# Kernel optimization log

Hardware: AMD Instinct MI355X
Metric: run time of the kernel (lower is better)

## Reference

```python
import jax, jax.numpy as jnp
import numpy as np

B, C, H, W = 2048, 512, 4, 4
T, D, NH, HD, FF, NL = 16, 512, 8, 64, 1024, 4
EPS = 1e-5
SCALE = float(1.0 / np.sqrt(HD))


def _make_adj(h, w):
    # torch_geometric.utils.grid(h, w): 3x3 neighborhood incl. self-loop;
    # GCNConv sym-normalizes: A_hat = D^-1/2 A D^-1/2
    n = h * w
    A = np.zeros((n, n), np.float32)
    for r in range(h):
        for c in range(w):
            for dr in (-1, 0, 1):
                for dc in (-1, 0, 1):
                    rr, cc = r + dr, c + dc
                    if 0 <= rr < h and 0 <= cc < w:
                        A[r * w + c, rr * w + cc] = 1.0
    dinv = 1.0 / np.sqrt(A.sum(1))
    return (A * dinv[:, None] * dinv[None, :]).astype(np.float32)


def setup_inputs():
    key = jax.random.key(0)
    ks = iter(jax.random.split(key, 64))
    def w(*s):
        return jax.random.normal(next(ks), s, jnp.float32) * 0.02
    return dict(
        x=jax.random.normal(next(ks), (B, C, H, W), jnp.float32),
        emb_w=w(D, D), emb_b=jnp.zeros((D,), jnp.float32),
        emb_ln_g=jnp.ones((D,), jnp.float32), emb_ln_b=jnp.zeros((D,), jnp.float32),
        pos=w(1, T, D),
        attn_wq=w(NL, D, D), attn_wk=w(NL, D, D), attn_wv=w(NL, D, D),
        attn_bq=jnp.zeros((NL, D), jnp.float32), attn_bk=jnp.zeros((NL, D), jnp.float32),
        attn_bv=jnp.zeros((NL, D), jnp.float32),
        attn_wo=w(NL, D, D), attn_bo=jnp.zeros((NL, D), jnp.float32),
        ln1_g=jnp.ones((NL, D), jnp.float32), ln1_b=jnp.zeros((NL, D), jnp.float32),
        ff_w1=w(NL, D, FF), ff_b1=jnp.zeros((NL, FF), jnp.float32),
        ff_w2=w(NL, FF, D), ff_b2=jnp.zeros((NL, D), jnp.float32),
        ln2_g=jnp.ones((NL, D), jnp.float32), ln2_b=jnp.zeros((NL, D), jnp.float32),
        fc_w=w(D, D), fc_b=jnp.zeros((D,), jnp.float32),
        fc_ln_g=jnp.ones((D,), jnp.float32), fc_ln_b=jnp.zeros((D,), jnp.float32),
        gcn_w1=w(C, 2 * C), gcn_b1=jnp.zeros((2 * C,), jnp.float32),
        gcn_ln1_g=jnp.ones((2 * C,), jnp.float32), gcn_ln1_b=jnp.zeros((2 * C,), jnp.float32),
        gcn_w2=w(2 * C, C), gcn_b2=jnp.zeros((C,), jnp.float32),
        gcn_ln2_g=jnp.ones((C,), jnp.float32), gcn_ln2_b=jnp.zeros((C,), jnp.float32),
        fusion_w=w(C, 2 * C), fusion_b=jnp.zeros((C,), jnp.float32),
        adj=jnp.asarray(_make_adj(H, W)),
    )


def _ln(x, g, b):
    mu = x.mean(-1, keepdims=True)
    var = ((x - mu) ** 2).mean(-1, keepdims=True)
    return (x - mu) * jax.lax.rsqrt(var + EPS) * g + b


def reference(x, emb_w, emb_b, emb_ln_g, emb_ln_b, pos,
              attn_wq, attn_wk, attn_wv, attn_bq, attn_bk, attn_bv, attn_wo, attn_bo,
              ln1_g, ln1_b, ff_w1, ff_b1, ff_w2, ff_b2, ln2_g, ln2_b,
              fc_w, fc_b, fc_ln_g, fc_ln_b,
              gcn_w1, gcn_b1, gcn_ln1_g, gcn_ln1_b, gcn_w2, gcn_b2, gcn_ln2_g, gcn_ln2_b,
              fusion_w, fusion_b, adj):
    Bx = x.shape[0]
    # ---- transformer branch: tokens = 16 spatial positions, dim 512 ----
    h = x.reshape(Bx, C, T).transpose(0, 2, 1)                 # [B,T,D]
    h = _ln(h @ emb_w + emb_b, emb_ln_g, emb_ln_b) + pos
    for i in range(NL):  # post-norm TransformerEncoderLayer, ReLU, eval (no dropout)
        q = (h @ attn_wq[i] + attn_bq[i]).reshape(Bx, T, NH, HD).transpose(0, 2, 1, 3)
        k = (h @ attn_wk[i] + attn_bk[i]).reshape(Bx, T, NH, HD).transpose(0, 2, 1, 3)
        v = (h @ attn_wv[i] + attn_bv[i]).reshape(Bx, T, NH, HD).transpose(0, 2, 1, 3)
        a = jax.nn.softmax(jnp.einsum('bhqd,bhkd->bhqk', q, k) * SCALE, axis=-1)
        o = jnp.einsum('bhqk,bhkd->bhqd', a, v).transpose(0, 2, 1, 3).reshape(Bx, T, D)
        h = _ln(h + o @ attn_wo[i] + attn_bo[i], ln1_g[i], ln1_b[i])
        f = jax.nn.relu(h @ ff_w1[i] + ff_b1[i]) @ ff_w2[i] + ff_b2[i]
        h = _ln(h + f, ln2_g[i], ln2_b[i])
    h = _ln(h @ fc_w + fc_b, fc_ln_g, fc_ln_b)
    x1 = h.transpose(0, 2, 1).reshape(Bx, C, H, W)
    # ---- GCN branch: dense normalized adjacency over the 16-node grid ----
    xn = x.transpose(0, 2, 3, 1).reshape(Bx, T, C)             # [B,16,C]
    g = jnp.einsum('mn,bnd->bmd', adj, xn @ gcn_w1) + gcn_b1   # GCNConv1 (bias after aggr)
    g = jax.nn.elu(_ln(g, gcn_ln1_g, gcn_ln1_b))
    g = jnp.einsum('mn,bnd->bmd', adj, g @ gcn_w2) + gcn_b2    # GCNConv2
    g = jax.nn.elu(_ln(g, gcn_ln2_g, gcn_ln2_b))
    x2 = g.reshape(Bx, H, W, C).transpose(0, 3, 1, 2)
    # ---- fusion: 1x1 conv + InstanceNorm2d (no affine) + ELU ----
    xc = jnp.concatenate([x1, x2], axis=1)                     # [B,2C,H,W]
    y = jnp.einsum('oc,bchw->bohw', fusion_w, xc) + fusion_b[None, :, None, None]
    mu = y.mean((2, 3), keepdims=True)
    var = ((y - mu) ** 2).mean((2, 3), keepdims=True)
    y = (y - mu) * jax.lax.rsqrt(var + EPS)
    return jax.nn.elu(y)
```

## Files before the change

### kernel.cpp

```cpp
#include <hip/hip_runtime.h>


typedef _Float16 f16;
typedef f16 f16x8 __attribute__((ext_vector_type(8)));
typedef f16 f16x4 __attribute__((ext_vector_type(4)));
typedef float f32x4 __attribute__((ext_vector_type(4)));

#define BM 128
#define BN 128
#define BK 32

__device__ inline float wred_sum(float s) {
#pragma unroll
  for (int m = 32; m; m >>= 1) s += __shfl_xor(s, m);
  return s;
}

struct WDesc {
  const float* src;
  f16* dst;
  int K, N, tiles_n, tile_base, mode;
};
struct WTable {
  WDesc d[32];
  int n;
};

__global__ void wconvert_kernel(WTable tab) {
  const int tile = blockIdx.x;
  int di = 0;
  while (di + 1 < tab.n && tab.d[di + 1].tile_base <= tile) ++di;
  const WDesc w = tab.d[di];
  const int t = tile - w.tile_base;
  const int tk = t / w.tiles_n, tn = t % w.tiles_n;
  const int tid = threadIdx.x;
  const int rr = tid >> 5, cc = tid & 31;
  __shared__ float tb[32][33];
  if (w.mode == 0) {
#pragma unroll
    for (int i = 0; i < 4; i++) {
      const int k = tk * 32 + i * 8 + rr, n = tn * 32 + cc;
      tb[i * 8 + rr][cc] = w.src[(size_t)k * w.N + n];
    }
    __syncthreads();
#pragma unroll
    for (int i = 0; i < 4; i++) {
      const int n = tn * 32 + i * 8 + rr, k = tk * 32 + cc;
      w.dst[(size_t)n * w.K + k] = (f16)tb[cc][i * 8 + rr];
    }
  } else {
#pragma unroll
    for (int i = 0; i < 4; i++) {
      const int k = tk * 32 + i * 8 + rr, n = tn * 32 + cc;
      w.dst[(size_t)k * w.N + n] = (f16)w.src[(size_t)k * w.N + n];
    }
  }
}

__global__ void biaspack_kernel(const float* __restrict__ bq,
                                const float* __restrict__ bk,
                                const float* __restrict__ bv,
                                float* __restrict__ bqkv) {
  const int i = blockIdx.x * 256 + threadIdx.x;
  if (i >= 4 * 1536) return;
  const int l = i / 1536, j = i % 1536;
  float v;
  if (j < 512)       v = bq[l * 512 + j];
  else if (j < 1024) v = bk[l * 512 + j - 512];
  else               v = bv[l * 512 + j - 1024];
  bqkv[i] = v;
}

__global__ void prep_kernel(const float* __restrict__ x, f16* __restrict__ X0) {
  const int b = blockIdx.x;
  for (int c = threadIdx.x; c < 512; c += 256) {
    const float* src = x + ((size_t)b * 512 + c) * 16;
    float vals[16];
#pragma unroll
    for (int i = 0; i < 4; i++) {
      const float4 v = ((const float4*)src)[i];
      vals[i * 4 + 0] = v.x; vals[i * 4 + 1] = v.y;
      vals[i * 4 + 2] = v.z; vals[i * 4 + 3] = v.w;
    }
#pragma unroll
    for (int t = 0; t < 16; t++)
      X0[((size_t)b * 16 + t) * 512 + c] = (f16)vals[t];
  }
}

template <int OUT, bool RELU, bool HASB>
__global__ __launch_bounds__(256) void gemm_kernel(
    const f16* __restrict__ A, const f16* __restrict__ Bt, void* __restrict__ C,
    const float* __restrict__ bias, int N, int K, int lda, int ldb) {
  __shared__ alignas(16) f16 sm[3][8192];
  const int tid = threadIdx.x;
  const int nb = N >> 7;
  const int cpx = gridDim.x >> 3;
  const int wg = (blockIdx.x & 7) * cpx + (blockIdx.x >> 3);
  const int bx = wg % nb;
  const int by = wg / nb;
  const int row0 = by << 7, col0 = bx << 7;
  const int lane = tid & 63;
  const int wave = tid >> 6;
  const int wm = (wave >> 1) << 6;
  const int wn = (wave & 1) << 6;
  const int srow = tid >> 2;
  const int schunk = (tid & 3) ^ ((tid >> 3) & 3);
  const f16* gA = A + (size_t)(row0 + srow) * lda + (schunk << 3);
  const f16* gB = Bt + (size_t)(col0 + srow) * ldb + (schunk << 3);
  const int wave_off = (tid & 0xC0) << 3;
  f32x4 acc[4][4] = {};
  const int rm = lane & 15;
  const int kg = lane >> 4;
  const int nt = K >> 5;

  auto STAGE = [&](int t, int bufi) {
    f16* lA = sm[bufi] + wave_off;
    f16* lB = sm[bufi] + 4096 + wave_off;
    const int kt = t << 5;
    __builtin_amdgcn_global_load_lds(
        (const __attribute__((address_space(1))) void*)(gA + kt),
        (__attribute__((address_space(3))) void*)lA, 16, 0, 0);
    __builtin_amdgcn_global_load_lds(
        (const __attribute__((address_space(1))) void*)(gA + (size_t)64 * lda + kt),
        (__attribute__((address_space(3))) void*)(lA + 2048), 16, 0, 0);
    __builtin_amdgcn_global_load_lds(
        (const __attribute__((address_space(1))) void*)(gB + kt),
        (__attribute__((address_space(3))) void*)lB, 16, 0, 0);
    __builtin_amdgcn_global_load_lds(
        (const __attribute__((address_space(1))) void*)(gB + (size_t)64 * ldb + kt),
        (__attribute__((address_space(3))) void*)(lB + 2048), 16, 0, 0);
  };

  STAGE(0, 0);
  STAGE(1, 1);
  asm volatile("s_waitcnt vmcnt(4)" ::: "memory");
  __builtin_amdgcn_s_barrier();

  for (int t = 0; t < nt; ++t) {
    const int cur = t % 3;
    if (t + 2 < nt) STAGE(t + 2, (t + 2) % 3);
    const f16* As = sm[cur];
    const f16* Bs = sm[cur] + 4096;
    f16x8 af[4], bf[4];
#pragma unroll
    for (int m = 0; m < 4; ++m) {
      const int r = wm + m * 16 + rm;
      af[m] = *(const f16x8*)(As + (r << 5) + ((kg ^ ((r >> 1) & 3)) << 3));
    }
#pragma unroll
    for (int n = 0; n < 4; ++n) {
      const int r = wn + n * 16 + rm;
      bf[n] = *(const f16x8*)(Bs + (r << 5) + ((kg ^ ((r >> 1) & 3)) << 3));
    }
#pragma unroll
    for (int m = 0; m < 4; ++m)
#pragma unroll
      for (int n = 0; n < 4; ++n)
        acc[m][n] =
            __builtin_amdgcn_mfma_f32_16x16x32_f16(af[m], bf[n], acc[m][n], 0, 0, 0);
    if (t + 2 < nt) {
      asm volatile("s_waitcnt vmcnt(4)" ::: "memory");
    } else {
      asm volatile("s_waitcnt vmcnt(0)" ::: "memory");
    }
    __builtin_amdgcn_s_barrier();
  }

  const int cn = lane & 15;
  const int rg = (lane >> 4) << 2;
#pragma unroll
  for (int m = 0; m < 4; ++m) {
#pragma unroll
    for (int n = 0; n < 4; ++n) {
      const int col = col0 + wn + n * 16 + cn;
      const float bv = HASB ? bias[col] : 0.0f;
#pragma unroll
      for (int r = 0; r < 4; ++r) {
        const int row = row0 + wm + m * 16 + rg + r;
        float v = acc[m][n][r] + bv;
        if (OUT == 2) v += ((float*)C)[(size_t)row * N + col];
        if (RELU) v = v > 0.f ? v : 0.f;
        if (OUT == 0)
          ((f16*)C)[(size_t)row * N + col] = (f16)v;
        else
          ((float*)C)[(size_t)row * N + col] = v;
      }
    }
  }
}

template <bool RES, bool POS>
__global__ void ln_kernel(const f16* in, const f16* res, const float* g,
                          const float* b, const float* pos, f16* out) {
  const int row = (blockIdx.x << 2) + (threadIdx.x >> 6);
  const int lane = threadIdx.x & 63;
  const int c0 = lane << 3;
  float v[8];
  const f16x8 xi = *(const f16x8*)(in + (size_t)row * 512 + c0);
  if (RES) {
    const f16x8 ri = *(const f16x8*)(res + (size_t)row * 512 + c0);
#pragma unroll
    for (int j = 0; j < 8; j++) v[j] = (float)xi[j] + (float)ri[j];
  } else {
#pragma unroll
    for (int j = 0; j < 8; j++) v[j] = (float)xi[j];
  }
  float s = 0;
#pragma unroll
  for (int j = 0; j < 8; j++) s += v[j];
  s = wred_sum(s);
  const float mu = s * (1.f / 512.f);
  float q = 0;
#pragma unroll
  for (int j = 0; j < 8; j++) {
    const float d = v[j] - mu;
    q += d * d;
  }
  q = wred_sum(q);
  const float rstd = rsqrtf(q * (1.f / 512.f) + 1e-5f);
  const int t = row & 15;
  f16x8 o8;
#pragma unroll
  for (int j = 0; j < 8; j++) {
    float o = (v[j] - mu) * rstd * g[c0 + j] + b[c0 + j];
    if (POS) o += pos[t * 512 + c0 + j];
    o8[j] = (f16)o;
  }
  *(f16x8*)(out + (size_t)row * 512 + c0) = o8;
}

__global__ __launch_bounds__(256) void attn_kernel(const f16* __restrict__ qkv,
                                                   f16* __restrict__ o) {
  __shared__ f16 smem[4][3776];
  const int wid = threadIdx.x >> 6;
  const int lane = threadIdx.x & 63;
  const int bh = (blockIdx.x << 2) + wid;
  const int b = bh >> 3, h = bh & 7;
  f16* W = smem[wid];
  f16* Qw = W;
  f16* Kw = W + 1152;
  f16* Vw = W + 2304;
  f16* Pw = W + 3456;
  const size_t base = (size_t)b * 24576 + (size_t)h * 64;
#pragma unroll
  for (int i = 0; i < 6; i++) {
    const int c = i * 64 + lane;
    const int t = c / 24;
    const int rem = c - t * 24;
    const int mat = rem >> 3, ch = rem & 7;
    const f16x8 v = *(const f16x8*)(qkv + base + (size_t)t * 1536 + mat * 512 + ch * 8);
    *(f16x8*)(W + mat * 1152 + t * 72 + ch * 8) = v;
  }
  __syncthreads();
  const int rm = lane & 15, kg = lane >> 4;
  f32x4 s4 = {};
  {
    const f16x8 q0 = *(const f16x8*)(Qw + rm * 72 + kg * 8);
    const f16x8 q1 = *(const f16x8*)(Qw + rm * 72 + 32 + kg * 8);
    const f16x8 k0 = *(const f16x8*)(Kw + rm * 72 + kg * 8);
    const f16x8 k1 = *(const f16x8*)(Kw + rm * 72 + 32 + kg * 8);
    s4 = __builtin_amdgcn_mfma_f32_16x16x32_f16(q0, k0, s4, 0, 0, 0);
    s4 = __builtin_amdgcn_mfma_f32_16x16x32_f16(q1, k1, s4, 0, 0, 0);
  }
  float p[4];
#pragma unroll
  for (int r = 0; r < 4; r++) {
    const float sv = s4[r] * 0.125f;
    float m = sv;
    m = fmaxf(m, __shfl_xor(m, 1));
    m = fmaxf(m, __shfl_xor(m, 2));
    m = fmaxf(m, __shfl_xor(m, 4));
    m = fmaxf(m, __shfl_xor(m, 8));
    const float e = expf(sv - m);
    float s = e;
    s += __shfl_xor(s, 1);
    s += __shfl_xor(s, 2);
    s += __shfl_xor(s, 4);
    s += __shfl_xor(s, 8);
    p[r] = e / s;
  }
#pragma unroll
  for (int r = 0; r < 4; r++) Pw[(kg * 4 + r) * 20 + rm] = (f16)p[r];
  __syncthreads();
  const f16x4 pa = *(const f16x4*)(Pw + rm * 20 + kg * 4);
  f32x4 o4[4] = {};
#pragma unroll
  for (int dt = 0; dt < 4; dt++) {
    f16x4 vb;
#pragma unroll
    for (int kk = 0; kk < 4; kk++) vb[kk] = Vw[(kg * 4 + kk) * 72 + dt * 16 + rm];
    o4[dt] = __builtin_amdgcn_mfma_f32_16x16x16f16(pa, vb, o4[dt], 0, 0, 0);
  }
  f16* op = o + (size_t)b * 16 * 512 + (size_t)h * 64;
#pragma unroll
  for (int dt = 0; dt < 4; dt++)
#pragma unroll
    for (int r = 0; r < 4; r++)
      op[(size_t)(kg * 4 + r) * 512 + dt * 16 + rm] = (f16)o4[dt][r];
}

template <int DG>
__global__ __launch_bounds__(256) void adjmix_kernel(
    const f16* __restrict__ r, const float* __restrict__ adj,
    const float* __restrict__ bias, const float* __restrict__ g,
    const float* __restrict__ bet, f16* __restrict__ out, int ldo) {
  const int b = blockIdx.x;
  const int tid = threadIdx.x;
  __shared__ float agg[16][DG];
  __shared__ float adjs[256];
  if (tid < 256) adjs[tid] = adj[tid];
  __syncthreads();
  const int d0 = tid * 4;
  if (d0 < DG) {
    float acc[16][4];
#pragma unroll
    for (int m = 0; m < 16; m++)
#pragma unroll
      for (int j = 0; j < 4; j++) acc[m][j] = 0.f;
#pragma unroll
    for (int n = 0; n < 16; n++) {
      const f16x4 v = *(const f16x4*)(r + ((size_t)b * 16 + n) * DG + d0);
      const float v0 = (float)v[0], v1 = (float)v[1], v2 = (float)v[2], v3 = (float)v[3];
#pragma unroll
      for (int m = 0; m < 16; m++) {
        const float a = adjs[m * 16 + n];
        acc[m][0] += a * v0;
        acc[m][1] += a * v1;
        acc[m][2] += a * v2;
        acc[m][3] += a * v3;
      }
    }
    const float4 bv = *(const float4*)(bias + d0);
#pragma unroll
    for (int m = 0; m < 16; m++) {
      agg[m][d0 + 0] = acc[m][0] + bv.x;
      agg[m][d0 + 1] = acc[m][1] + bv.y;
      agg[m][d0 + 2] = acc[m][2] + bv.z;
      agg[m][d0 + 3] = acc[m][3] + bv.w;
    }
  }
  __syncthreads();
  const int wave = tid >> 6, lane = tid & 63;
  for (int m = wave; m < 16; m += 4) {
    float s = 0;
#pragma unroll
    for (int j = 0; j < DG / 64; j++) s += agg[m][j * 64 + lane];
    s = wred_sum(s);
    const float mu = s / DG;
    float q = 0;
#pragma unroll
    for (int j = 0; j < DG / 64; j++) {
      const float t = agg[m][j * 64 + lane] - mu;
      q += t * t;
    }
    q = wred_sum(q);
    const float rstd = rsqrtf(q / DG + 1e-5f);
    const size_t grow = (size_t)b * 16 + m;
#pragma unroll
    for (int j = 0; j < DG / 64; j++) {
      const int d = j * 64 + lane;
      float v = (agg[m][d] - mu) * rstd * g[d] + bet[d];
      v = v > 0.f ? v : expm1f(v);
      out[grow * ldo + d] = (f16)v;
    }
  }
}

__global__ void instnorm_kernel(const float* __restrict__ y, float* __restrict__ out) {
  const int b = blockIdx.x;
  for (int oc = threadIdx.x; oc < 512; oc += 256) {
    float v[16];
    float s = 0;
#pragma unroll
    for (int t = 0; t < 16; t++) {
      v[t] = y[((size_t)b * 16 + t) * 512 + oc];
      s += v[t];
    }
    const float mu = s * (1.f / 16.f);
    float q = 0;
#pragma unroll
    for (int t = 0; t < 16; t++) {
      const float d = v[t] - mu;
      q += d * d;
    }
    const float rstd = rsqrtf(q * (1.f / 16.f) + 1e-5f);
    float* op = out + ((size_t)b * 512 + oc) * 16;
#pragma unroll
    for (int t = 0; t < 16; t++) {
      const float z = (v[t] - mu) * rstd;
      op[t] = z > 0.f ? z : expm1f(z);
    }
  }
}

extern "C" void kernel_launch(void* const* d_in, const int* in_sizes, int n_in,
                              void* d_out, int out_size, void* d_ws, size_t ws_size,
                              hipStream_t stream) {
  (void)in_sizes; (void)n_in; (void)out_size; (void)ws_size;
  const float* x         = (const float*)d_in[0];
  const float* emb_w     = (const float*)d_in[1];
  const float* emb_b     = (const float*)d_in[2];
  const float* emb_ln_g  = (const float*)d_in[3];
  const float* emb_ln_b  = (const float*)d_in[4];
  const float* pos       = (const float*)d_in[5];
  const float* attn_wq   = (const float*)d_in[6];
  const float* attn_wk   = (const float*)d_in[7];
  const float* attn_wv   = (const float*)d_in[8];
  const float* attn_bq   = (const float*)d_in[9];
  const float* attn_bk   = (const float*)d_in[10];
  const float* attn_bv   = (const float*)d_in[11];
  const float* attn_wo   = (const float*)d_in[12];
  const float* attn_bo   = (const float*)d_in[13];
  const float* ln1_g     = (const float*)d_in[14];
  const float* ln1_b     = (const float*)d_in[15];
  const float* ff_w1     = (const float*)d_in[16];
  const float* ff_b1     = (const float*)d_in[17];
  const float* ff_w2     = (const float*)d_in[18];
  const float* ff_b2     = (const float*)d_in[19];
  const float* ln2_g     = (const float*)d_in[20];
  const float* ln2_b     = (const float*)d_in[21];
  const float* fc_w      = (const float*)d_in[22];
  const float* fc_b      = (const float*)d_in[23];
  const float* fc_ln_g   = (const float*)d_in[24];
  const float* fc_ln_b   = (const float*)d_in[25];
  const float* gcn_w1    = (const float*)d_in[26];
  const float* gcn_b1    = (const float*)d_in[27];
  const float* gcn_ln1_g = (const float*)d_in[28];
  const float* gcn_ln1_b = (const float*)d_in[29];
  const float* gcn_w2    = (const float*)d_in[30];
  const float* gcn_b2    = (const float*)d_in[31];
  const float* gcn_ln2_g = (const float*)d_in[32];
  const float* gcn_ln2_b = (const float*)d_in[33];
  const float* fusion_w  = (const float*)d_in[34];
  const float* fusion_b  = (const float*)d_in[35];
  const float* adj       = (const float*)d_in[36];

  char* ws = (char*)d_ws;
  f16*   WF   = (f16*)(ws);
  float* BQKV = (float*)(ws + 20971520ull);
  f16*   Ap   = (f16*)(ws + 20996096ull);
  f16*   Bp   = (f16*)(ws + 54550528ull);
  f16*   Cp   = (f16*)(ws + 88104960ull);
  f16*   Qp   = (f16*)(ws + 121659392ull);

  const size_t o_emb = 0, o_qkv = 262144, o_wo = 3407872, o_ff1 = 4456448,
               o_ff2 = 6553600, o_fc = 8650752, o_g1 = 8912896, o_g2 = 9437184,
               o_fus = 9961472;

  WTable tab{};
  int ntab = 0, tbase = 0;
  auto add = [&](const float* s, f16* dst, int K, int N, int mode) {
    WDesc& w = tab.d[ntab++];
    w.src = s; w.dst = dst; w.K = K; w.N = N;
    w.tiles_n = N / 32; w.tile_base = tbase; w.mode = mode;
    tbase += (K / 32) * (N / 32);
  };
  add(emb_w, WF + o_emb, 512, 512, 0);
  for (int l = 0; l < 4; l++) {
    add(attn_wq + l * 262144, WF + o_qkv + (size_t)l * 786432, 512, 512, 0);
    add(attn_wk + l * 262144, WF + o_qkv + (size_t)l * 786432 + 262144, 512, 512, 0);
    add(attn_wv + l * 262144, WF + o_qkv + (size_t)l * 786432 + 524288, 512, 512, 0);
  }
  for (int l = 0; l < 4; l++)
    add(attn_wo + l * 262144, WF + o_wo + (size_t)l * 262144, 512, 512, 0);
  for (int l = 0; l < 4; l++)
    add(ff_w1 + l * 524288, WF + o_ff1 + (size_t)l * 524288, 512, 1024, 0);
  for (int l = 0; l < 4; l++)
    add(ff_w2 + l * 524288, WF + o_ff2 + (size_t)l * 524288, 1024, 512, 0);
  add(fc_w, WF + o_fc, 512, 512, 0);
  add(gcn_w1, WF + o_g1, 512, 1024, 0);
  add(gcn_w2, WF + o_g2, 1024, 512, 0);
  add(fusion_w, WF + o_fus, 512, 1024, 1);
  tab.n = ntab;

  wconvert_kernel<<<tbase, 256, 0, stream>>>(tab);
  biaspack_kernel<<<24, 256, 0, stream>>>(attn_bq, attn_bk, attn_bv, BQKV);
  prep_kernel<<<2048, 256, 0, stream>>>(x, Ap);

  gemm_kernel<0, false, false><<<256 * 8, 256, 0, stream>>>(
      Ap, WF + o_g1, Qp, nullptr, 1024, 512, 512, 512);
  adjmix_kernel<1024><<<2048, 256, 0, stream>>>(
      Qp, adj, gcn_b1, gcn_ln1_g, gcn_ln1_b, Bp, 1024);
  gemm_kernel<0, false, false><<<256 * 4, 256, 0, stream>>>(
      Bp, WF + o_g2, Qp, nullptr, 512, 1024, 1024, 1024);

  gemm_kernel<0, false, true><<<256 * 4, 256, 0, stream>>>(
      Ap, WF + o_emb, Cp, emb_b, 512, 512, 512, 512);
  ln_kernel<false, true><<<8192, 256, 0, stream>>>(
      Cp, nullptr, emb_ln_g, emb_ln_b, pos, Bp);

  adjmix_kernel<512><<<2048, 256, 0, stream>>>(
      Qp, adj, gcn_b2, gcn_ln2_g, gcn_ln2_b, Ap, 512);

  for (int i = 0; i < 4; i++) {
    gemm_kernel<0, false, true><<<256 * 12, 256, 0, stream>>>(
        Bp, WF + o_qkv + (size_t)i * 786432, Qp, BQKV + i * 1536, 1536, 512, 512, 512);
    attn_kernel<<<4096, 256, 0, stream>>>(Qp, Cp);
    gemm_kernel<0, false, true><<<256 * 4, 256, 0, stream>>>(
        Cp, WF + o_wo + (size_t)i * 262144, Qp, attn_bo + i * 512, 512, 512, 512, 512);
    ln_kernel<true, false><<<8192, 256, 0, stream>>>(
        Qp, Bp, ln1_g + i * 512, ln1_b + i * 512, nullptr, Bp);
    gemm_kernel<0, true, true><<<256 * 8, 256, 0, stream>>>(
        Bp, WF + o_ff1 + (size_t)i * 524288, Qp, ff_b1 + i * 1024, 1024, 512, 512, 512);
    gemm_kernel<0, false, true><<<256 * 4, 256, 0, stream>>>(
        Qp, WF + o_ff2 + (size_t)i * 524288, Qp + 33554432ull, ff_b2 + i * 512,
        512, 1024, 1024, 1024);
    ln_kernel<true, false><<<8192, 256, 0, stream>>>(
        Qp + 33554432ull, Bp, ln2_g + i * 512, ln2_b + i * 512, nullptr, Bp);
  }

  gemm_kernel<0, false, true><<<256 * 4, 256, 0, stream>>>(
      Bp, WF + o_fc, Cp, fc_b, 512, 512, 512, 512);
  ln_kernel<false, false><<<8192, 256, 0, stream>>>(
      Cp, nullptr, fc_ln_g, fc_ln_b, nullptr, Cp);

  float* Yf = (float*)Qp;
  gemm_kernel<1, false, true><<<256 * 4, 256, 0, stream>>>(
      Cp, WF + o_fus, Yf, fusion_b, 512, 512, 512, 1024);
  gemm_kernel<2, false, false><<<256 * 4, 256, 0, stream>>>(
      Ap, WF + o_fus + 512, Yf, nullptr, 512, 512, 512, 1024);

  instnorm_kernel<<<2048, 256, 0, stream>>>(Yf, (float*)d_out);
}
```

Measured before the change: 1.437 ms.

## Fuse fusion GEMMs into one K=1024 GEMM with instance-norm ELU epilogue

The final LayerNorm now writes the transformer output and the GCN output side by side into one packed [rows,1024] f16 buffer. This lets the two accumulating fusion GEMMs become a single GEMM with K=1024. A new epilogue mode computes the per-batch 16-token instance norm and ELU directly from the accumulators using lane shuffles, then writes the output layout with float4 stores. The separate instnorm kernel and the fp32 intermediate round trip go away. The fusion bias is dropped, which is exact because instance norm removes any per-channel constant, but the epilogue relies on each 16-row MFMA tile mapping to exactly one batch.

Result: faster. 1.335 ms (-7.2%).

```diff
diff --git a/kernel.cpp b/kernel.cpp
--- a/kernel.cpp
+++ b/kernel.cpp
@@ -5,10 +5,6 @@
 typedef f16 f16x8 __attribute__((ext_vector_type(8)));
 typedef f16 f16x4 __attribute__((ext_vector_type(4)));
 typedef float f32x4 __attribute__((ext_vector_type(4)));
-
-#define BM 128
-#define BN 128
-#define BK 32
 
 __device__ inline float wred_sum(float s) {
 #pragma unroll
@@ -169,22 +165,47 @@
 
   const int cn = lane & 15;
   const int rg = (lane >> 4) << 2;
-#pragma unroll
-  for (int m = 0; m < 4; ++m) {
-#pragma unroll
-    for (int n = 0; n < 4; ++n) {
-      const int col = col0 + wn + n * 16 + cn;
-      const float bv = HASB ? bias[col] : 0.0f;
-#pragma unroll
-      for (int r = 0; r < 4; ++r) {
-        const int row = row0 + wm + m * 16 + rg + r;
-        float v = acc[m][n][r] + bv;
-        if (OUT == 2) v += ((float*)C)[(size_t)row * N + col];
-        if (RELU) v = v > 0.f ? v : 0.f;
-        if (OUT == 0)
+  if (OUT == 3) {
+    float* out = (float*)C;
+#pragma unroll
+    for (int m = 0; m < 4; ++m) {
+      const int bidx = (row0 >> 4) + (wm >> 4) + m;
+#pragma unroll
+      for (int n = 0; n < 4; ++n) {
+        const int col = col0 + wn + n * 16 + cn;
+        const float v0 = acc[m][n][0], v1 = acc[m][n][1];
+        const float v2 = acc[m][n][2], v3 = acc[m][n][3];
+        float s = v0 + v1 + v2 + v3;
+        s += __shfl_xor(s, 16);
+        s += __shfl_xor(s, 32);
+        const float mu = s * (1.f / 16.f);
+        float q = (v0 - mu) * (v0 - mu) + (v1 - mu) * (v1 - mu) +
+                  (v2 - mu) * (v2 - mu) + (v3 - mu) * (v3 - mu);
+        q += __shfl_xor(q, 16);
+        q += __shfl_xor(q, 32);
+        const float rstd = rsqrtf(q * (1.f / 16.f) + 1e-5f);
+        float4 z;
+        z.x = (v0 - mu) * rstd; z.x = z.x > 0.f ? z.x : expm1f(z.x);
+        z.y = (v1 - mu) * rstd; z.y = z.y > 0.f ? z.y : expm1f(z.y);
+        z.z = (v2 - mu) * rstd; z.z = z.z > 0.f ? z.z : expm1f(z.z);
+        z.w = (v3 - mu) * rstd; z.w = z.w > 0.f ? z.w : expm1f(z.w);
+        *(float4*)(out + ((size_t)bidx * 512 + col) * 16 + rg) = z;
+      }
+    }
+  } else {
+#pragma unroll
+    for (int m = 0; m < 4; ++m) {
+#pragma unroll
+      for (int n = 0; n < 4; ++n) {
+        const int col = col0 + wn + n * 16 + cn;
+        const float bv = HASB ? bias[col] : 0.0f;
+#pragma unroll
+        for (int r = 0; r < 4; ++r) {
+          const int row = row0 + wm + m * 16 + rg + r;
+          float v = acc[m][n][r] + bv;
+          if (RELU) v = v > 0.f ? v : 0.f;
           ((f16*)C)[(size_t)row * N + col] = (f16)v;
-        else
-          ((float*)C)[(size_t)row * N + col] = v;
+        }
       }
     }
   }
@@ -228,6 +249,38 @@
     o8[j] = (f16)o;
   }
   *(f16x8*)(out + (size_t)row * 512 + c0) = o8;
+}
+
+__global__ void lnpack_kernel(const f16* __restrict__ in, const f16* __restrict__ x2,
+                              const float* __restrict__ g, const float* __restrict__ b,
+                              f16* __restrict__ F) {
+  const int row = (blockIdx.x << 2) + (threadIdx.x >> 6);
+  const int lane = threadIdx.x & 63;
+  const int c0 = lane << 3;
+  const f16x8 xi = *(const f16x8*)(in + (size_t)row * 512 + c0);
+  float v[8];
+#pragma unroll
+  for (int j = 0; j < 8; j++) v[j] = (float)xi[j];
+  float s = 0;
+#pragma unroll
+  for (int j = 0; j < 8; j++) s += v[j];
+  s = wred_sum(s);
+  const float mu = s * (1.f / 512.f);
+  float q = 0;
+#pragma unroll
+  for (int j = 0; j < 8; j++) {
+    const float d = v[j] - mu;
+    q += d * d;
+  }
+  q = wred_sum(q);
+  const float rstd = rsqrtf(q * (1.f / 512.f) + 1e-5f);
+  f16x8 o8;
+#pragma unroll
+  for (int j = 0; j < 8; j++)
+    o8[j] = (f16)((v[j] - mu) * rstd * g[c0 + j] + b[c0 + j]);
+  *(f16x8*)(F + (size_t)row * 1024 + c0) = o8;
+  const f16x8 x2v = *(const f16x8*)(x2 + (size_t)row * 512 + c0);
+  *(f16x8*)(F + (size_t)row * 1024 + 512 + c0) = x2v;
 }
 
 __global__ __launch_bounds__(256) void attn_kernel(const f16* __restrict__ qkv,
@@ -363,33 +416,6 @@
       float v = (agg[m][d] - mu) * rstd * g[d] + bet[d];
       v = v > 0.f ? v : expm1f(v);
       out[grow * ldo + d] = (f16)v;
-    }
-  }
-}
-
-__global__ void instnorm_kernel(const float* __restrict__ y, float* __restrict__ out) {
-  const int b = blockIdx.x;
-  for (int oc = threadIdx.x; oc < 512; oc += 256) {
-    float v[16];
-    float s = 0;
-#pragma unroll
-    for (int t = 0; t < 16; t++) {
-      v[t] = y[((size_t)b * 16 + t) * 512 + oc];
-      s += v[t];
-    }
-    const float mu = s * (1.f / 16.f);
-    float q = 0;
-#pragma unroll
-    for (int t = 0; t < 16; t++) {
-      const float d = v[t] - mu;
-      q += d * d;
-    }
-    const float rstd = rsqrtf(q * (1.f / 16.f) + 1e-5f);
-    float* op = out + ((size_t)b * 512 + oc) * 16;
-#pragma unroll
-    for (int t = 0; t < 16; t++) {
-      const float z = (v[t] - mu) * rstd;
-      op[t] = z > 0.f ? z : expm1f(z);
     }
   }
 }
@@ -435,6 +461,7 @@
   const float* fusion_w  = (const float*)d_in[34];
   const float* fusion_b  = (const float*)d_in[35];
   const float* adj       = (const float*)d_in[36];
+  (void)fusion_b;
 
   char* ws = (char*)d_ws;
   f16*   WF   = (f16*)(ws);
@@ -511,15 +538,9 @@
   }
 
   gemm_kernel<0, false, true><<<256 * 4, 256, 0, stream>>>(
-      Bp, WF + o_fc, Cp, fc_b, 512, 512, 512, 512);
-  ln_kernel<false, false><<<8192, 256, 0, stream>>>(
-      Cp, nullptr, fc_ln_g, fc_ln_b, nullptr, Cp);
-
-  float* Yf = (float*)Qp;
-  gemm_kernel<1, false, true><<<256 * 4, 256, 0, stream>>>(
-      Cp, WF + o_fus, Yf, fusion_b, 512, 512, 512, 1024);
-  gemm_kernel<2, false, false><<<256 * 4, 256, 0, stream>>>(
-      Ap, WF + o_fus + 512, Yf, nullptr, 512, 512, 512, 1024);
-
-  instnorm_kernel<<<2048, 256, 0, stream>>>(Yf, (float*)d_out);
-}
+      Bp, WF + o_fc, Qp, fc_b, 512, 512, 512, 512);
+  lnpack_kernel<<<8192, 256, 0, stream>>>(Qp, Ap, fc_ln_g, fc_ln_b, Bp);
+
+  gemm_kernel<3, false, false><<<256 * 4, 256, 0, stream>>>(
+      Bp, WF + o_fus, d_out, nullptr, 512, 1024, 1024, 1024);
+}
```
